# Performance work log

Hardware: AMD Instinct MI355X
Metric: run time of the kernel (lower is better)

The kernel has to match this reference:

```python
import jax, jax.numpy as jnp
import numpy as np

# --- constants from init_kwargs ---
nx, NX, dx, nt, dt = 256, 512, 1e-4, 256, 2e-5
nm, sr, sR = 256, 4, 200
fc, sgma, t0, bg = 500.0, 1e-3, 2e-3, 1.5

_times = np.arange(nt, dtype=np.float32) * dt
SRC = (np.sin(2.0 * np.pi * fc * _times) * np.exp(-(_times - t0) ** 2 / (2.0 * sgma ** 2))).astype(np.float32)  # [nt]
_thetas = 2.0 * np.pi * np.arange(nm) / nm
_mx = (NX / 2 + sR * np.cos(_thetas)).astype(int)
_my = (NX / 2 + sR * np.sin(_thetas)).astype(int)
MEAS = jnp.asarray(NX * _mx + _my)          # [nm]  flat receiver indices
TRANS = jnp.asarray((NX * _mx + _my)[::sr])  # [nr]  flat transmitter indices
nr = TRANS.shape[0]
abc_pd = NX // 2 - sR - 1                    # 55
pd = (NX - nx) // 2 - abc_pd                 # 73
SRC_COEF = (bg * dt / dx) ** 2               # 0.09


def _forward(x, se):
    # pad imaging region with background speed, then absorbing rim with ~0 speed
    xp = jnp.pad(x, ((0, 0), (0, 0), (pd, pd), (pd, pd)), constant_values=bg)
    xp = jnp.pad(xp, ((0, 0), (0, 0), (abc_pd, abc_pd), (abc_pd, abc_pd)), constant_values=1e-6)
    vel2 = (dt * xp / dx) ** 2               # [B,C,NX,NX], constant over time
    B, C = xp.shape[0], xp.shape[1]

    def step(carry, src_j):
        p0, p1 = carry
        # 4th-order periodic (roll-based) Laplacian, matching torch.roll semantics
        nab_x = (-jnp.roll(p1, 2, -2) + 16 * jnp.roll(p1, 1, -2) - 30 * p1
                 + 16 * jnp.roll(p1, -1, -2) - jnp.roll(p1, -2, -2)) / 12
        nab_y = (-jnp.roll(p1, 2, -1) + 16 * jnp.roll(p1, 1, -1) - 30 * p1
                 + 16 * jnp.roll(p1, -1, -1) - jnp.roll(p1, -2, -1)) / 12
        p = 2 * p1 - p0 + vel2 * (nab_x + nab_y)
        pf = p.reshape(B, C, NX * NX)
        # scatter source injection at transmitter pixels (indices are unique)
        pf = pf.at[:, :, TRANS].set(pf[:, :, TRANS] + SRC_COEF * src_j * se[None, None, :])
        meas = pf[:, :, MEAS]                # gather receivers [B,C,nm]
        return (p1, pf.reshape(B, C, NX, NX)), meas

    zeros = jnp.zeros_like(xp)
    _, ys = jax.lax.scan(step, (zeros, zeros), jnp.asarray(SRC))
    return jnp.moveaxis(ys, 0, -1)           # [B,C,nm,nt]


def setup_inputs():
    key = jax.random.key(0)
    k1, k2 = jax.random.split(key)
    x = 1.4 + 0.2 * jax.random.uniform(k1, (4, 1, nx, nx), dtype=jnp.float32)  # sound-speed map
    se = jax.random.normal(k2, (nr,), dtype=jnp.float32)                       # source encoding weights
    return {"x": x, "se": se}


def reference(x, se):
    return _forward(x, se)
```

## Files before the change

kernel.cpp:

```cpp
#include <hip/hip_runtime.h>
#include <math.h>
#include <string.h>

#define NXG 512
#define NPTS (NXG * NXG)
#define NB 4
#define NT 256
#define NM 256
#define K 16
#define NCH (NT / K)
#define WROWS 128
#define WCOLS 128
#define NTHR 1024
#define NTILES 64
#define LROWS 136

__device__ __forceinline__ float dpp_left(float v) {
    return __int_as_float(__builtin_amdgcn_mov_dpp(__float_as_int(v),
                                                   0x138, 0xf, 0xf, true));
}
__device__ __forceinline__ float dpp_right(float v) {
    return __int_as_float(__builtin_amdgcn_mov_dpp(__float_as_int(v),
                                                   0x130, 0xf, 0xf, true));
}

__device__ __forceinline__ void row_calc(
    const float (&cur)[4][4], float (&dst)[4][4],
    const float (&v2R)[4][4], int r,
    const float* __restrict__ xm2, const float* __restrict__ xm1,
    const float* __restrict__ xp1, const float* __restrict__ xp2)
{
    float y[8] = {dpp_left(cur[r][2]), dpp_left(cur[r][3]),
                  cur[r][0], cur[r][1], cur[r][2], cur[r][3],
                  dpp_right(cur[r][0]), dpp_right(cur[r][1])};
#pragma unroll
    for (int c = 0; c < 4; ++c) {
        float cc = cur[r][c];
        float sum1 = (xm1[c] + xp1[c]) + (y[c + 1] + y[c + 3]);
        float sum2 = (xm2[c] + xp2[c]) + (y[c] + y[c + 4]);
        float w = fmaf(-60.0f, cc, fmaf(16.0f, sum1, -sum2));
        dst[r][c] = fmaf(v2R[r][c], w, fmaf(2.0f, cc, -dst[r][c]));
    }
}

__device__ __forceinline__ void do_step(
    const float* __restrict__ Lc, float* __restrict__ Ln,
    const float (&v2R)[4][4], float (&cur)[4][4], float (&nw)[4][4],
    int base, int c0)
{
    float4 a4 = *(const float4*)&Lc[(base - 2) * WCOLS + c0];
    float4 b4 = *(const float4*)&Lc[(base - 1) * WCOLS + c0];
    float4 c4 = *(const float4*)&Lc[(base + 4) * WCOLS + c0];
    float4 d4 = *(const float4*)&Lc[(base + 5) * WCOLS + c0];

    float ha[4] = {a4.x, a4.y, a4.z, a4.w};
    float hb[4] = {b4.x, b4.y, b4.z, b4.w};
    row_calc(cur, nw, v2R, 0, ha, hb, cur[1], cur[2]);
    *(float4*)&Ln[(base + 0) * WCOLS + c0] =
        make_float4(nw[0][0], nw[0][1], nw[0][2], nw[0][3]);
    row_calc(cur, nw, v2R, 1, hb, cur[0], cur[2], cur[3]);
    *(float4*)&Ln[(base + 1) * WCOLS + c0] =
        make_float4(nw[1][0], nw[1][1], nw[1][2], nw[1][3]);

    float hc[4] = {c4.x, c4.y, c4.z, c4.w};
    float hd[4] = {d4.x, d4.y, d4.z, d4.w};
    row_calc(cur, nw, v2R, 2, cur[0], cur[1], cur[3], hc);
    *(float4*)&Ln[(base + 2) * WCOLS + c0] =
        make_float4(nw[2][0], nw[2][1], nw[2][2], nw[2][3]);
    row_calc(cur, nw, v2R, 3, cur[1], cur[2], hc, hd);
    *(float4*)&Ln[(base + 3) * WCOLS + c0] =
        make_float4(nw[3][0], nw[3][1], nw[3][2], nw[3][3]);
}

__device__ __forceinline__ void patch_step(
    float (&f)[4][4], float* __restrict__ Ln, float* __restrict__ out,
    int base, int c0, int injCell, float addv,
    int m1Cell, int m1Addr, int m2Cell, int m2Addr, int n)
{
    if (injCell >= 0) {
#pragma unroll
        for (int r = 0; r < 4; ++r)
#pragma unroll
            for (int c = 0; c < 4; ++c)
                if (((r << 2) | c) == injCell) f[r][c] += addv;
        int ir = injCell >> 2;
        if (ir == 0) *(float4*)&Ln[(base + 0) * WCOLS + c0] = make_float4(f[0][0], f[0][1], f[0][2], f[0][3]);
        if (ir == 1) *(float4*)&Ln[(base + 1) * WCOLS + c0] = make_float4(f[1][0], f[1][1], f[1][2], f[1][3]);
        if (ir == 2) *(float4*)&Ln[(base + 2) * WCOLS + c0] = make_float4(f[2][0], f[2][1], f[2][2], f[2][3]);
        if (ir == 3) *(float4*)&Ln[(base + 3) * WCOLS + c0] = make_float4(f[3][0], f[3][1], f[3][2], f[3][3]);
    }
    if (m1Cell >= 0) {
        float v = 0.0f;
#pragma unroll
        for (int r = 0; r < 4; ++r)
#pragma unroll
            for (int c = 0; c < 4; ++c)
                if (((r << 2) | c) == m1Cell) v = f[r][c];
        out[m1Addr | n] = v;
    }
    if (m2Cell >= 0) {
        float v = 0.0f;
#pragma unroll
        for (int r = 0; r < 4; ++r)
#pragma unroll
            for (int c = 0; c < 4; ++c)
                if (((r << 2) | c) == m2Cell) v = f[r][c];
        out[m2Addr | n] = v;
    }
}

__global__ __launch_bounds__(NTHR, 4) void chunk_kernel(
    const float* __restrict__ x,
    const float* __restrict__ se,
    float* __restrict__ out,
    const float* __restrict__ gA,
    const float* __restrict__ gB,
    float* __restrict__ wA,
    float* __restrict__ wB,
    float* __restrict__ vel2,
    const int2* __restrict__ thrTab,
    const float* __restrict__ srcT,
    int n0)
{
    __shared__ __align__(16) float L0[LROWS * WCOLS];
    __shared__ __align__(16) float L1[LROWS * WCOLS];

    const int tid = threadIdx.x;
    const int blk = blockIdx.x;
    const int b   = blk >> 6;
    const int tb  = blk & 63;
    const int gi0 = (tb >> 3) << 6;
    const int gj0 = (tb & 7) << 6;
    const int bi0 = gi0 - 32;
    const int bj0 = gj0 - 32;

    const int grp = tid >> 5;
    const int r0  = grp << 2;
    const int c0  = (tid & 31) << 2;
    const int base = (grp + 1) << 2;

    const bool wbT = (r0 >= 32 && r0 < 96 && c0 >= 32 && c0 < 96);

    float curR[4][4], prvR[4][4], v2R[4][4];
    if (n0 == 0) {
#pragma unroll
        for (int r = 0; r < 4; ++r) {
            int gi = (bi0 + r0 + r) & 511;
            int gjb = (bj0 + c0) & 511;
#pragma unroll
            for (int c = 0; c < 4; ++c) {
                int gj = gjb + c;
                float v;
                if (gi < 55 || gi >= 457 || gj < 55 || gj >= 457) v = 1e-6f;
                else if (gi >= 128 && gi < 384 && gj >= 128 && gj < 384)
                    v = x[(b << 16) | ((gi - 128) << 8) | (gj - 128)];
                else v = 1.5f;
                float a = (2e-05f * v) / 1e-04f;
                v2R[r][c] = a * a * (1.0f / 12.0f);
                curR[r][c] = 0.0f;
                prvR[r][c] = 0.0f;
            }
        }
        if (wbT) {
            int gj = gj0 + (c0 - 32);
#pragma unroll
            for (int r = 0; r < 4; ++r) {
                int gi = gi0 + (r0 - 32) + r;
                *(float4*)&vel2[(b << 18) | (gi << 9) | gj] =
                    make_float4(v2R[r][0], v2R[r][1], v2R[r][2], v2R[r][3]);
            }
        }
    } else {
        const float* gAb = gA + (b << 18);
        const float* gBb = gB + (b << 18);
        const float* gVb = vel2 + (b << 18);
#pragma unroll
        for (int r = 0; r < 4; ++r) {
            int gi = (bi0 + r0 + r) & 511;
            int gj = (bj0 + c0) & 511;
            float4 cv = *(const float4*)&gAb[(gi << 9) | gj];
            float4 pv = *(const float4*)&gBb[(gi << 9) | gj];
            float4 vv = *(const float4*)&gVb[(gi << 9) | gj];
            curR[r][0] = cv.x; curR[r][1] = cv.y; curR[r][2] = cv.z; curR[r][3] = cv.w;
            prvR[r][0] = pv.x; prvR[r][1] = pv.y; prvR[r][2] = pv.z; prvR[r][3] = pv.w;
            v2R[r][0] = vv.x; v2R[r][1] = vv.y; v2R[r][2] = vv.z; v2R[r][3] = vv.w;
        }
    }

    const int2 tw = thrTab[(tb << 10) | tid];
    int injCell = -1;  float injV = 0.0f;
    if (tw.x >= 0) { injCell = tw.x & 15; injV = 0.09f * se[tw.x >> 8]; }
    int m1Cell = -1, m1Addr = 0, m2Cell = -1, m2Addr = 0;
    {
        int h1 = tw.y & 0xFFFF, h2 = (tw.y >> 16) & 0xFFFF;
        if (h1 & 0x8000) { m1Cell = (h1 >> 8) & 15; m1Addr = (b << 16) | ((h1 & 255) << 8); }
        if (h2 & 0x8000) { m2Cell = (h2 >> 8) & 15; m2Addr = (b << 16) | ((h2 & 255) << 8); }
    }
    const bool rare = (injCell >= 0) || (m1Cell >= 0) || (m2Cell >= 0);

    *(float4*)&L0[(base + 0) * WCOLS + c0] = make_float4(curR[0][0], curR[0][1], curR[0][2], curR[0][3]);
    *(float4*)&L0[(base + 1) * WCOLS + c0] = make_float4(curR[1][0], curR[1][1], curR[1][2], curR[1][3]);
    *(float4*)&L0[(base + 2) * WCOLS + c0] = make_float4(curR[2][0], curR[2][1], curR[2][2], curR[2][3]);
    *(float4*)&L0[(base + 3) * WCOLS + c0] = make_float4(curR[3][0], curR[3][1], curR[3][2], curR[3][3]);
    __syncthreads();

#pragma unroll 1
    for (int s = 0; s < K; s += 2) {
        float sva = srcT[n0 + s];
        float svb = srcT[n0 + s + 1];

        do_step(L0, L1, v2R, curR, prvR, base, c0);
        if (rare) patch_step(prvR, L1, out, base, c0, injCell, injV * sva,
                             m1Cell, m1Addr, m2Cell, m2Addr, n0 + s);
        __syncthreads();

        do_step(L1, L0, v2R, prvR, curR, base, c0);
        if (rare) patch_step(curR, L0, out, base, c0, injCell, injV * svb,
                             m1Cell, m1Addr, m2Cell, m2Addr, n0 + s + 1);
        if (s + 2 < K) __syncthreads();
    }

    if (wbT) {
        int gj = gj0 + (c0 - 32);
#pragma unroll
        for (int r = 0; r < 4; ++r) {
            int gi = gi0 + (r0 - 32) + r;
            *(float4*)&wA[(b << 18) | (gi << 9) | gj] =
                make_float4(curR[r][0], curR[r][1], curR[r][2], curR[r][3]);
            *(float4*)&wB[(b << 18) | (gi << 9) | gj] =
                make_float4(prvR[r][0], prvR[r][1], prvR[r][2], prvR[r][3]);
        }
    }
}

extern "C" void kernel_launch(void* const* d_in, const int* in_sizes, int n_in,
                              void* d_out, int out_size, void* d_ws, size_t ws_size,
                              hipStream_t stream) {
    const float* x  = (const float*)d_in[0];
    const float* se = (const float*)d_in[1];
    float* out = (float*)d_out;

    float* ws = (float*)d_ws;
    const int FSZ = NB * NPTS;
    float* f[4]  = {ws, ws + FSZ, ws + 2 * FSZ, ws + 3 * FSZ};
    float* dVel  = ws + 4 * FSZ;
    int*   dBlob = (int*)(ws + 5 * FSZ);
    int2*  dTT   = (int2*)dBlob;
    float* dSrc  = (float*)(dBlob + NTILES * NTHR * 2);

    static int h_blob[NTILES * NTHR * 2 + NT];
    int*   h_tt  = h_blob;
    static float h_src[NT];
    static int h_mx[NM], h_my[NM];
    for (int m = 0; m < NM; ++m) {
        double theta = (2.0 * M_PI * (double)m) / 256.0;
        h_mx[m] = (int)(256.0 + 200.0 * cos(theta));
        h_my[m] = (int)(256.0 + 200.0 * sin(theta));
    }
    for (int i = 0; i < NTILES * NTHR; ++i) { h_tt[2*i] = -1; h_tt[2*i+1] = 0; }
    for (int tile = 0; tile < NTILES; ++tile) {
        int bi0 = ((tile >> 3) << 6) - 32;
        int bj0 = ((tile & 7) << 6) - 32;
        for (int m = 0; m < NM; ++m) {
            int d = (h_mx[m] - bi0) & 511;
            int e = (h_my[m] - bj0) & 511;
            if (d >= WROWS || e >= WCOLS) continue;
            int tidx = (d >> 2) * 32 + (e >> 2);
            int cell = ((d & 3) << 2) | (e & 3);
            int basei = (tile * NTHR + tidx) * 2;
            if ((m & 3) == 0) h_tt[basei] = ((m >> 2) << 8) | cell;
            if (d >= 32 && d < 96 && e >= 32 && e < 96) {
                int pk = 0x8000 | (cell << 8) | m;
                if (!(h_tt[basei + 1] & 0x8000)) h_tt[basei + 1] |= pk;
                else                             h_tt[basei + 1] |= pk << 16;
            }
        }
    }
    for (int t = 0; t < NT; ++t) {
        float tj  = (float)t * 2e-05f;
        float arg = (float)(2.0 * M_PI * 500.0) * tj;
        float d   = tj - 0.002f;
        float e   = -(d * d) / (float)(2.0 * 0.001 * 0.001);
        h_src[t]  = sinf(arg) * expf(e);
    }
    memcpy(&h_blob[NTILES * NTHR * 2], h_src, sizeof(h_src));
    hipMemcpyAsync(dBlob, h_blob, sizeof(h_blob), hipMemcpyHostToDevice, stream);

    for (int c = 0; c < NCH; ++c) {
        int p = c & 1, q = p ^ 1;
        chunk_kernel<<<NB * NTILES, NTHR, 0, stream>>>(
            x, se, out,
            f[2 * p], f[2 * p + 1],
            f[2 * q], f[2 * q + 1],
            dVel, dTT, dSrc, c * K);
    }
}
```

Measured before the change: 724.5 us.

## Fuse all time chunks into one persistent cooperative kernel with grid sync

```diff
diff --git a/kernel.cpp b/kernel.cpp
--- a/kernel.cpp
+++ b/kernel.cpp
@@ -1,6 +1,9 @@
 #include <hip/hip_runtime.h>
+#include <hip/hip_cooperative_groups.h>
 #include <math.h>
 #include <string.h>
+
+namespace cg = cooperative_groups;
 
 #define NXG 512
 #define NPTS (NXG * NXG)
@@ -109,18 +112,14 @@
     }
 }
 
-__global__ __launch_bounds__(NTHR, 4) void chunk_kernel(
+__global__ __launch_bounds__(NTHR, 4) void wave_kernel(
     const float* __restrict__ x,
     const float* __restrict__ se,
     float* __restrict__ out,
-    const float* __restrict__ gA,
-    const float* __restrict__ gB,
-    float* __restrict__ wA,
-    float* __restrict__ wB,
-    float* __restrict__ vel2,
+    float* __restrict__ f0A, float* __restrict__ f0B,
+    float* __restrict__ f1A, float* __restrict__ f1B,
     const int2* __restrict__ thrTab,
-    const float* __restrict__ srcT,
-    int n0)
+    const float* __restrict__ srcT)
 {
     __shared__ __align__(16) float L0[LROWS * WCOLS];
     __shared__ __align__(16) float L1[LROWS * WCOLS];
@@ -142,48 +141,22 @@
     const bool wbT = (r0 >= 32 && r0 < 96 && c0 >= 32 && c0 < 96);
 
     float curR[4][4], prvR[4][4], v2R[4][4];
-    if (n0 == 0) {
-#pragma unroll
-        for (int r = 0; r < 4; ++r) {
-            int gi = (bi0 + r0 + r) & 511;
-            int gjb = (bj0 + c0) & 511;
-#pragma unroll
-            for (int c = 0; c < 4; ++c) {
-                int gj = gjb + c;
-                float v;
-                if (gi < 55 || gi >= 457 || gj < 55 || gj >= 457) v = 1e-6f;
-                else if (gi >= 128 && gi < 384 && gj >= 128 && gj < 384)
-                    v = x[(b << 16) | ((gi - 128) << 8) | (gj - 128)];
-                else v = 1.5f;
-                float a = (2e-05f * v) / 1e-04f;
-                v2R[r][c] = a * a * (1.0f / 12.0f);
-                curR[r][c] = 0.0f;
-                prvR[r][c] = 0.0f;
-            }
-        }
-        if (wbT) {
-            int gj = gj0 + (c0 - 32);
-#pragma unroll
-            for (int r = 0; r < 4; ++r) {
-                int gi = gi0 + (r0 - 32) + r;
-                *(float4*)&vel2[(b << 18) | (gi << 9) | gj] =
-                    make_float4(v2R[r][0], v2R[r][1], v2R[r][2], v2R[r][3]);
-            }
-        }
-    } else {
-        const float* gAb = gA + (b << 18);
-        const float* gBb = gB + (b << 18);
-        const float* gVb = vel2 + (b << 18);
-#pragma unroll
-        for (int r = 0; r < 4; ++r) {
-            int gi = (bi0 + r0 + r) & 511;
-            int gj = (bj0 + c0) & 511;
-            float4 cv = *(const float4*)&gAb[(gi << 9) | gj];
-            float4 pv = *(const float4*)&gBb[(gi << 9) | gj];
-            float4 vv = *(const float4*)&gVb[(gi << 9) | gj];
-            curR[r][0] = cv.x; curR[r][1] = cv.y; curR[r][2] = cv.z; curR[r][3] = cv.w;
-            prvR[r][0] = pv.x; prvR[r][1] = pv.y; prvR[r][2] = pv.z; prvR[r][3] = pv.w;
-            v2R[r][0] = vv.x; v2R[r][1] = vv.y; v2R[r][2] = vv.z; v2R[r][3] = vv.w;
+#pragma unroll
+    for (int r = 0; r < 4; ++r) {
+        int gi = (bi0 + r0 + r) & 511;
+        int gjb = (bj0 + c0) & 511;
+#pragma unroll
+        for (int c = 0; c < 4; ++c) {
+            int gj = gjb + c;
+            float v;
+            if (gi < 55 || gi >= 457 || gj < 55 || gj >= 457) v = 1e-6f;
+            else if (gi >= 128 && gi < 384 && gj >= 128 && gj < 384)
+                v = x[(b << 16) | ((gi - 128) << 8) | (gj - 128)];
+            else v = 1.5f;
+            float a = (2e-05f * v) / 1e-04f;
+            v2R[r][c] = a * a * (1.0f / 12.0f);
+            curR[r][c] = 0.0f;
+            prvR[r][c] = 0.0f;
         }
     }
 
@@ -198,37 +171,62 @@
     }
     const bool rare = (injCell >= 0) || (m1Cell >= 0) || (m2Cell >= 0);
 
-    *(float4*)&L0[(base + 0) * WCOLS + c0] = make_float4(curR[0][0], curR[0][1], curR[0][2], curR[0][3]);
-    *(float4*)&L0[(base + 1) * WCOLS + c0] = make_float4(curR[1][0], curR[1][1], curR[1][2], curR[1][3]);
-    *(float4*)&L0[(base + 2) * WCOLS + c0] = make_float4(curR[2][0], curR[2][1], curR[2][2], curR[2][3]);
-    *(float4*)&L0[(base + 3) * WCOLS + c0] = make_float4(curR[3][0], curR[3][1], curR[3][2], curR[3][3]);
-    __syncthreads();
+    cg::grid_group grid = cg::this_grid();
 
 #pragma unroll 1
-    for (int s = 0; s < K; s += 2) {
-        float sva = srcT[n0 + s];
-        float svb = srcT[n0 + s + 1];
-
-        do_step(L0, L1, v2R, curR, prvR, base, c0);
-        if (rare) patch_step(prvR, L1, out, base, c0, injCell, injV * sva,
-                             m1Cell, m1Addr, m2Cell, m2Addr, n0 + s);
+    for (int ch = 0; ch < NCH; ++ch) {
+        const int n0 = ch * K;
+
+        *(float4*)&L0[(base + 0) * WCOLS + c0] = make_float4(curR[0][0], curR[0][1], curR[0][2], curR[0][3]);
+        *(float4*)&L0[(base + 1) * WCOLS + c0] = make_float4(curR[1][0], curR[1][1], curR[1][2], curR[1][3]);
+        *(float4*)&L0[(base + 2) * WCOLS + c0] = make_float4(curR[2][0], curR[2][1], curR[2][2], curR[2][3]);
+        *(float4*)&L0[(base + 3) * WCOLS + c0] = make_float4(curR[3][0], curR[3][1], curR[3][2], curR[3][3]);
         __syncthreads();
 
-        do_step(L1, L0, v2R, prvR, curR, base, c0);
-        if (rare) patch_step(curR, L0, out, base, c0, injCell, injV * svb,
-                             m1Cell, m1Addr, m2Cell, m2Addr, n0 + s + 1);
-        if (s + 2 < K) __syncthreads();
-    }
-
-    if (wbT) {
-        int gj = gj0 + (c0 - 32);
-#pragma unroll
-        for (int r = 0; r < 4; ++r) {
-            int gi = gi0 + (r0 - 32) + r;
-            *(float4*)&wA[(b << 18) | (gi << 9) | gj] =
-                make_float4(curR[r][0], curR[r][1], curR[r][2], curR[r][3]);
-            *(float4*)&wB[(b << 18) | (gi << 9) | gj] =
-                make_float4(prvR[r][0], prvR[r][1], prvR[r][2], prvR[r][3]);
+#pragma unroll 1
+        for (int s = 0; s < K; s += 2) {
+            float sva = srcT[n0 + s];
+            float svb = srcT[n0 + s + 1];
+
+            do_step(L0, L1, v2R, curR, prvR, base, c0);
+            if (rare) patch_step(prvR, L1, out, base, c0, injCell, injV * sva,
+                                 m1Cell, m1Addr, m2Cell, m2Addr, n0 + s);
+            __syncthreads();
+
+            do_step(L1, L0, v2R, prvR, curR, base, c0);
+            if (rare) patch_step(curR, L0, out, base, c0, injCell, injV * svb,
+                                 m1Cell, m1Addr, m2Cell, m2Addr, n0 + s + 1);
+            if (s + 2 < K) __syncthreads();
+        }
+
+        if (ch + 1 < NCH) {
+            float* bA = (ch & 1) ? f1A : f0A;
+            float* bB = (ch & 1) ? f1B : f0B;
+            if (wbT) {
+                int gj = gj0 + (c0 - 32);
+#pragma unroll
+                for (int r = 0; r < 4; ++r) {
+                    int gi = gi0 + (r0 - 32) + r;
+                    *(float4*)&bA[(b << 18) | (gi << 9) | gj] =
+                        make_float4(curR[r][0], curR[r][1], curR[r][2], curR[r][3]);
+                    *(float4*)&bB[(b << 18) | (gi << 9) | gj] =
+                        make_float4(prvR[r][0], prvR[r][1], prvR[r][2], prvR[r][3]);
+                }
+            }
+            grid.sync();
+            if (!wbT) {
+                const float* gAb = bA + (b << 18);
+                const float* gBb = bB + (b << 18);
+#pragma unroll
+                for (int r = 0; r < 4; ++r) {
+                    int gi = (bi0 + r0 + r) & 511;
+                    int gj = (bj0 + c0) & 511;
+                    float4 cv = *(const float4*)&gAb[(gi << 9) | gj];
+                    float4 pv = *(const float4*)&gBb[(gi << 9) | gj];
+                    curR[r][0] = cv.x; curR[r][1] = cv.y; curR[r][2] = cv.z; curR[r][3] = cv.w;
+                    prvR[r][0] = pv.x; prvR[r][1] = pv.y; prvR[r][2] = pv.z; prvR[r][3] = pv.w;
+                }
+            }
         }
     }
 }
@@ -242,9 +240,11 @@
 
     float* ws = (float*)d_ws;
     const int FSZ = NB * NPTS;
-    float* f[4]  = {ws, ws + FSZ, ws + 2 * FSZ, ws + 3 * FSZ};
-    float* dVel  = ws + 4 * FSZ;
-    int*   dBlob = (int*)(ws + 5 * FSZ);
+    float* f0A = ws;
+    float* f0B = ws + FSZ;
+    float* f1A = ws + 2 * FSZ;
+    float* f1B = ws + 3 * FSZ;
+    int*   dBlob = (int*)(ws + 4 * FSZ);
     int2*  dTT   = (int2*)dBlob;
     float* dSrc  = (float*)(dBlob + NTILES * NTHR * 2);
 
@@ -286,12 +286,10 @@
     memcpy(&h_blob[NTILES * NTHR * 2], h_src, sizeof(h_src));
     hipMemcpyAsync(dBlob, h_blob, sizeof(h_blob), hipMemcpyHostToDevice, stream);
 
-    for (int c = 0; c < NCH; ++c) {
-        int p = c & 1, q = p ^ 1;
-        chunk_kernel<<<NB * NTILES, NTHR, 0, stream>>>(
-            x, se, out,
-            f[2 * p], f[2 * p + 1],
-            f[2 * q], f[2 * q + 1],
-            dVel, dTT, dSrc, c * K);
-    }
-}
+    void* kargs[] = {(void*)&x, (void*)&se, (void*)&out,
+                     (void*)&f0A, (void*)&f0B, (void*)&f1A, (void*)&f1B,
+                     (void*)&dTT, (void*)&dSrc};
+    hipLaunchCooperativeKernel((void*)wave_kernel,
+                               dim3(NB * NTILES), dim3(NTHR),
+                               kargs, 0, stream);
+}
```

Result: slower. 1.024 ms (+41.3%).

## Skip halo rows per step, recompute vel2 in-kernel, drop final writeback

Applied to the files above, without the earlier changes.

```diff
diff --git a/kernel.cpp b/kernel.cpp
--- a/kernel.cpp
+++ b/kernel.cpp
@@ -117,7 +117,6 @@
     const float* __restrict__ gB,
     float* __restrict__ wA,
     float* __restrict__ wB,
-    float* __restrict__ vel2,
     const int2* __restrict__ thrTab,
     const float* __restrict__ srcT,
     int n0)
@@ -138,52 +137,50 @@
     const int r0  = grp << 2;
     const int c0  = (tid & 31) << 2;
     const int base = (grp + 1) << 2;
+    const int wr0 = (tid >> 6) << 3;
 
     const bool wbT = (r0 >= 32 && r0 < 96 && c0 >= 32 && c0 < 96);
 
     float curR[4][4], prvR[4][4], v2R[4][4];
-    if (n0 == 0) {
+    {
+        const int gjb = (bj0 + c0) & 511;
+        const bool colIn = (gjb >= 128 && gjb < 384);
 #pragma unroll
         for (int r = 0; r < 4; ++r) {
             int gi = (bi0 + r0 + r) & 511;
-            int gjb = (bj0 + c0) & 511;
+            bool rowPhys = (gi >= 55 && gi < 457);
+            bool inX = rowPhys && colIn && (gi >= 128 && gi < 384);
+            float4 xv = make_float4(1.5f, 1.5f, 1.5f, 1.5f);
+            if (inX) xv = *(const float4*)&x[(b << 16) | ((gi - 128) << 8) | (gjb - 128)];
+            float xa[4] = {xv.x, xv.y, xv.z, xv.w};
 #pragma unroll
             for (int c = 0; c < 4; ++c) {
                 int gj = gjb + c;
                 float v;
-                if (gi < 55 || gi >= 457 || gj < 55 || gj >= 457) v = 1e-6f;
-                else if (gi >= 128 && gi < 384 && gj >= 128 && gj < 384)
-                    v = x[(b << 16) | ((gi - 128) << 8) | (gj - 128)];
+                if (!rowPhys || gj < 55 || gj >= 457) v = 1e-6f;
+                else if (inX) v = xa[c];
                 else v = 1.5f;
                 float a = (2e-05f * v) / 1e-04f;
                 v2R[r][c] = a * a * (1.0f / 12.0f);
-                curR[r][c] = 0.0f;
-                prvR[r][c] = 0.0f;
             }
         }
-        if (wbT) {
-            int gj = gj0 + (c0 - 32);
-#pragma unroll
-            for (int r = 0; r < 4; ++r) {
-                int gi = gi0 + (r0 - 32) + r;
-                *(float4*)&vel2[(b << 18) | (gi << 9) | gj] =
-                    make_float4(v2R[r][0], v2R[r][1], v2R[r][2], v2R[r][3]);
-            }
-        }
+    }
+    if (n0 == 0) {
+#pragma unroll
+        for (int r = 0; r < 4; ++r)
+#pragma unroll
+            for (int c = 0; c < 4; ++c) { curR[r][c] = 0.0f; prvR[r][c] = 0.0f; }
     } else {
         const float* gAb = gA + (b << 18);
         const float* gBb = gB + (b << 18);
-        const float* gVb = vel2 + (b << 18);
 #pragma unroll
         for (int r = 0; r < 4; ++r) {
             int gi = (bi0 + r0 + r) & 511;
             int gj = (bj0 + c0) & 511;
             float4 cv = *(const float4*)&gAb[(gi << 9) | gj];
             float4 pv = *(const float4*)&gBb[(gi << 9) | gj];
-            float4 vv = *(const float4*)&gVb[(gi << 9) | gj];
             curR[r][0] = cv.x; curR[r][1] = cv.y; curR[r][2] = cv.z; curR[r][3] = cv.w;
             prvR[r][0] = pv.x; prvR[r][1] = pv.y; prvR[r][2] = pv.z; prvR[r][3] = pv.w;
-            v2R[r][0] = vv.x; v2R[r][1] = vv.y; v2R[r][2] = vv.z; v2R[r][3] = vv.w;
         }
     }
 
@@ -208,19 +205,27 @@
     for (int s = 0; s < K; s += 2) {
         float sva = srcT[n0 + s];
         float svb = srcT[n0 + s + 1];
-
-        do_step(L0, L1, v2R, curR, prvR, base, c0);
-        if (rare) patch_step(prvR, L1, out, base, c0, injCell, injV * sva,
-                             m1Cell, m1Addr, m2Cell, m2Addr, n0 + s);
+        int mA = 30 - 2 * s;
+        int mB = mA - 2;
+        bool actA = (wr0 + 7 >= 32 - mA) && (wr0 <= 95 + mA);
+        bool actB = (wr0 + 7 >= 32 - mB) && (wr0 <= 95 + mB);
+
+        if (actA) {
+            do_step(L0, L1, v2R, curR, prvR, base, c0);
+            if (rare) patch_step(prvR, L1, out, base, c0, injCell, injV * sva,
+                                 m1Cell, m1Addr, m2Cell, m2Addr, n0 + s);
+        }
         __syncthreads();
 
-        do_step(L1, L0, v2R, prvR, curR, base, c0);
-        if (rare) patch_step(curR, L0, out, base, c0, injCell, injV * svb,
-                             m1Cell, m1Addr, m2Cell, m2Addr, n0 + s + 1);
+        if (actB) {
+            do_step(L1, L0, v2R, prvR, curR, base, c0);
+            if (rare) patch_step(curR, L0, out, base, c0, injCell, injV * svb,
+                                 m1Cell, m1Addr, m2Cell, m2Addr, n0 + s + 1);
+        }
         if (s + 2 < K) __syncthreads();
     }
 
-    if (wbT) {
+    if (wbT && (n0 + K < NT)) {
         int gj = gj0 + (c0 - 32);
 #pragma unroll
         for (int r = 0; r < 4; ++r) {
@@ -243,8 +248,7 @@
     float* ws = (float*)d_ws;
     const int FSZ = NB * NPTS;
     float* f[4]  = {ws, ws + FSZ, ws + 2 * FSZ, ws + 3 * FSZ};
-    float* dVel  = ws + 4 * FSZ;
-    int*   dBlob = (int*)(ws + 5 * FSZ);
+    int*   dBlob = (int*)(ws + 4 * FSZ);
     int2*  dTT   = (int2*)dBlob;
     float* dSrc  = (float*)(dBlob + NTILES * NTHR * 2);
 
@@ -292,6 +296,6 @@
             x, se, out,
             f[2 * p], f[2 * p + 1],
             f[2 * q], f[2 * q + 1],
-            dVel, dTT, dSrc, c * K);
-    }
-}
+            dTT, dSrc, c * K);
+    }
+}
```

Measured after the change: 718.0 us. About the same (-0.9%).
